# Performance work log

Hardware: AMD Instinct MI355X
Metric: run time of the kernel (lower is better)

Reference implementation:

```python
import jax, jax.numpy as jnp
import numpy as np

N_RAYS = 262144
N_BINS = 64          # bin edges per ray
N_IMPORTANCE = 128   # fine samples per ray


def setup_inputs() -> dict:
    key = jax.random.key(0)
    k1, k2, k3 = jax.random.split(key, 3)
    # bins must be sorted along last axis (bin edges): cumsum of positive steps
    steps = jax.random.uniform(k1, (N_RAYS, N_BINS), dtype=jnp.float32) + 0.01
    bins = jnp.cumsum(steps, axis=-1)
    weights = jax.random.uniform(k2, (N_RAYS, N_BINS - 1), dtype=jnp.float32)
    # u plays the role of torch.rand t_vals (deterministic=False path)
    u = jax.random.uniform(k3, (N_RAYS, N_IMPORTANCE), dtype=jnp.float32)
    return {"bins": bins, "weights": weights, "u": u, "n_importance": N_IMPORTANCE}


def reference(bins, weights, u, n_importance):
    # weights: [N, M-1]; bins: [N, M]; u: [N, n_importance]
    weights = weights + 1e-5
    pdf = weights / jnp.sum(weights, axis=-1, keepdims=True)
    cdf = jnp.cumsum(pdf, axis=-1)
    cdf = jnp.concatenate([jnp.zeros_like(cdf[..., :1]), cdf], axis=-1)  # [N, M]

    # batched binary search (torch.searchsorted, right=False -> side='left')
    idx = jax.vmap(lambda c, t: jnp.searchsorted(c, t, side='left'))(
        jax.lax.stop_gradient(cdf), u)                                   # [N, I]
    lower = jnp.maximum(idx - 1, 0)
    upper = jnp.minimum(idx, cdf.shape[-1] - 1)

    cdf_lo = jnp.take_along_axis(cdf, lower, axis=-1)
    cdf_hi = jnp.take_along_axis(cdf, upper, axis=-1)
    bins_lo = jnp.take_along_axis(bins, lower, axis=-1)
    bins_hi = jnp.take_along_axis(bins, upper, axis=-1)

    denom = cdf_hi - cdf_lo
    denom = jnp.where(denom < 1e-5, jnp.ones_like(denom), denom)
    t = (u - cdf_lo) / denom
    samples = bins_lo + t * (bins_hi - bins_lo)                          # [N, I]
    return samples
```

## Files before the change

### kernel.cpp

```cpp
#include <hip/hip_runtime.h>


constexpr int NBINS = 64;
constexpr int NW = NBINS - 1;
constexpr int NIMP = 128;
constexpr int RAYS_PER_BLOCK = 4;

__global__ __launch_bounds__(256) void sample_pdf_kernel(
    const float* __restrict__ bins,
    const float* __restrict__ weights,
    const float* __restrict__ u,
    float* __restrict__ out,
    int n_rays)
{
    __shared__ float s_cdf[RAYS_PER_BLOCK][NBINS];
    __shared__ float s_bins[RAYS_PER_BLOCK][NBINS];

    const int wave = threadIdx.x >> 6;
    const int lane = threadIdx.x & 63;
    int ray = blockIdx.x * RAYS_PER_BLOCK + wave;
    if (ray >= n_rays) ray = n_rays - 1;

    s_bins[wave][lane] = bins[(size_t)ray * NBINS + lane];

    float v = (lane < NW) ? (weights[(size_t)ray * NW + lane] + 1e-5f) : 0.0f;
    #pragma unroll
    for (int off = 1; off < 64; off <<= 1) {
        const float n = __shfl_up(v, off, 64);
        if (lane >= off) v += n;
    }
    const float T = __shfl(v, NW - 1, 64);
    if (lane < NW) s_cdf[wave][lane + 1] = v / T;
    if (lane == 0) s_cdf[wave][0] = 0.0f;

    __syncthreads();

    const float* __restrict__ cdf = s_cdf[wave];
    const float* __restrict__ bn  = s_bins[wave];

    const float2 uu = ((const float2*)(u + (size_t)ray * NIMP))[lane];
    float2 res;

    #pragma unroll
    for (int k = 0; k < 2; ++k) {
        const float uv = (k == 0) ? uu.x : uu.y;

        int pos = 0;
        #pragma unroll
        for (int s = 32; s > 0; s >>= 1) {
            const int np = pos + s;
            if (cdf[np] < uv) pos = np;
        }
        const int idx   = (cdf[0] < uv) ? pos + 1 : 0;
        const int lower = (idx > 0) ? idx - 1 : 0;
        const int upper = (idx < NBINS - 1) ? idx : NBINS - 1;

        const float clo = cdf[lower], chi = cdf[upper];
        const float blo = bn[lower],  bhi = bn[upper];
        float denom = chi - clo;
        denom = (denom < 1e-5f) ? 1.0f : denom;
        const float t  = (uv - clo) / denom;
        const float sm = blo + t * (bhi - blo);
        if (k == 0) res.x = sm; else res.y = sm;
    }

    ((float2*)(out + (size_t)ray * NIMP))[lane] = res;
}

extern "C" void kernel_launch(void* const* d_in, const int* in_sizes, int n_in,
                              void* d_out, int out_size, void* d_ws, size_t ws_size,
                              hipStream_t stream) {
    const float* bins    = (const float*)d_in[0];
    const float* weights = (const float*)d_in[1];
    const float* u       = (const float*)d_in[2];
    float* out = (float*)d_out;

    const int n_rays = in_sizes[0] / NBINS;
    const int grid = (n_rays + RAYS_PER_BLOCK - 1) / RAYS_PER_BLOCK;
    sample_pdf_kernel<<<grid, 256, 0, stream>>>(bins, weights, u, out, n_rays);
}
```

Measured before the change: 330.7 us.

## Use DPP scan, readlane-based top search levels, and drop block barrier

Replaces the shuffle-based prefix sum with a DPP row/broadcast inclusive scan and readlane for the total. The first three binary-search levels now use CDF values broadcast from lanes 7 to 55, which leaves only three LDS probes. The __syncthreads is removed because each wave only reads its own shared slice, and the lower-side cdf value is carried through the search rather than re-read. The intent is to cut LDS latency and ds_bpermute traffic in a latency-bound kernel. Correctness now depends on in-order LDS access within a wave without an explicit barrier.

```diff
diff --git a/kernel.cpp b/kernel.cpp
--- a/kernel.cpp
+++ b/kernel.cpp
@@ -5,6 +5,26 @@
 constexpr int NW = NBINS - 1;
 constexpr int NIMP = 128;
 constexpr int RAYS_PER_BLOCK = 4;
+
+template <int Ctrl, int Rm>
+__device__ __forceinline__ float dppterm(float x) {
+    return __int_as_float(__builtin_amdgcn_update_dpp(
+        0, __float_as_int(x), Ctrl, Rm, 0xF, true));
+}
+
+__device__ __forceinline__ float rdlane(float x, int lane) {
+    return __int_as_float(__builtin_amdgcn_readlane(__float_as_int(x), lane));
+}
+
+__device__ __forceinline__ float wave_incl_scan(float x) {
+    x += dppterm<0x111, 0xF>(x);
+    x += dppterm<0x112, 0xF>(x);
+    x += dppterm<0x114, 0xF>(x);
+    x += dppterm<0x118, 0xF>(x);
+    x += dppterm<0x142, 0xA>(x);
+    x += dppterm<0x143, 0xC>(x);
+    return x;
+}
 
 __global__ __launch_bounds__(256) void sample_pdf_kernel(
     const float* __restrict__ bins,
@@ -21,19 +41,24 @@
     int ray = blockIdx.x * RAYS_PER_BLOCK + wave;
     if (ray >= n_rays) ray = n_rays - 1;
 
-    s_bins[wave][lane] = bins[(size_t)ray * NBINS + lane];
+    const float bv = bins[(size_t)ray * NBINS + lane];
+    s_bins[wave][lane] = bv;
 
-    float v = (lane < NW) ? (weights[(size_t)ray * NW + lane] + 1e-5f) : 0.0f;
-    #pragma unroll
-    for (int off = 1; off < 64; off <<= 1) {
-        const float n = __shfl_up(v, off, 64);
-        if (lane >= off) v += n;
-    }
-    const float T = __shfl(v, NW - 1, 64);
-    if (lane < NW) s_cdf[wave][lane + 1] = v / T;
-    if (lane == 0) s_cdf[wave][0] = 0.0f;
+    const float w = (lane < NW) ? (weights[(size_t)ray * NW + lane] + 1e-5f) : 0.0f;
+    const float S = wave_incl_scan(w);
+    const float T = rdlane(S, NW - 1);
+    const float cdfv = S / T;
 
-    __syncthreads();
+    if (lane < NW) s_cdf[wave][lane + 1] = cdfv;
+    if (lane == NW) s_cdf[wave][0] = 0.0f;
+
+    const float c8  = rdlane(cdfv, 7);
+    const float c16 = rdlane(cdfv, 15);
+    const float c24 = rdlane(cdfv, 23);
+    const float c32 = rdlane(cdfv, 31);
+    const float c40 = rdlane(cdfv, 39);
+    const float c48 = rdlane(cdfv, 47);
+    const float c56 = rdlane(cdfv, 55);
 
     const float* __restrict__ cdf = s_cdf[wave];
     const float* __restrict__ bn  = s_bins[wave];
@@ -46,20 +71,30 @@
         const float uv = (k == 0) ? uu.x : uu.y;
 
         int pos = 0;
+        float lo = 0.0f;
+        const bool b1 = (c32 < uv);
+        if (b1) { pos = 32; lo = c32; }
+        const float m2 = b1 ? c48 : c16;
+        const bool b2 = (m2 < uv);
+        if (b2) { pos += 16; lo = m2; }
+        const float m3 = b2 ? (b1 ? c56 : c24) : (b1 ? c40 : c8);
+        const bool b3 = (m3 < uv);
+        if (b3) { pos += 8; lo = m3; }
+
         #pragma unroll
-        for (int s = 32; s > 0; s >>= 1) {
-            const int np = pos + s;
-            if (cdf[np] < uv) pos = np;
+        for (int s = 4; s >= 1; s >>= 1) {
+            const float val = cdf[pos + s];
+            if (val < uv) { pos += s; lo = val; }
         }
-        const int idx   = (cdf[0] < uv) ? pos + 1 : 0;
-        const int lower = (idx > 0) ? idx - 1 : 0;
-        const int upper = (idx < NBINS - 1) ? idx : NBINS - 1;
 
-        const float clo = cdf[lower], chi = cdf[upper];
-        const float blo = bn[lower],  bhi = bn[upper];
-        float denom = chi - clo;
+        const int upper = (uv > 0.0f) ? (pos + 1) : 0;
+        const float chi = cdf[upper];
+        const float blo = bn[pos];
+        const float bhi = bn[upper];
+
+        float denom = chi - lo;
         denom = (denom < 1e-5f) ? 1.0f : denom;
-        const float t  = (uv - clo) / denom;
+        const float t = (uv - lo) / denom;
         const float sm = blo + t * (bhi - blo);
         if (k == 0) res.x = sm; else res.y = sm;
     }
```

Measured after the change: 325.3 us. About the same (-1.6%).
